# Kernel tuning notes

Measured on AMD Instinct MI355X. Metric: run time of the kernel, lower is better.

The kernel has to match this reference:

```python
import jax, jax.numpy as jnp
import numpy as np


def setup_inputs() -> dict:
    key = jax.random.key(0)
    k1, k2, k3 = jax.random.split(key, 3)
    B, C, D, H, W = 4, 64, 32, 64, 64
    x = jax.random.normal(k1, (B, C, D, H, W), dtype=jnp.float32)
    # Conv3d(in=2, out=1, k=7), PyTorch default init: U(-s, s), s = 1/sqrt(fan_in)
    fan_in = 2 * 7 * 7 * 7
    s = 1.0 / np.sqrt(fan_in)
    conv_w = jax.random.uniform(k2, (1, 2, 7, 7, 7), dtype=jnp.float32, minval=-s, maxval=s)
    conv_b = jax.random.uniform(k3, (1,), dtype=jnp.float32, minval=-s, maxval=s)
    return {"x": x, "conv_w": conv_w, "conv_b": conv_b}


def reference(x, conv_w, conv_b):
    # channel-wise max and mean -> [B, 2, D, H, W]
    xc = jnp.stack([jnp.max(x, axis=1), jnp.mean(x, axis=1)], axis=1)
    # conv3d 2->1, k7, stride 1, padding 3 (SAME)
    y = jax.lax.conv_general_dilated(
        xc, conv_w,
        window_strides=(1, 1, 1),
        padding=[(3, 3), (3, 3), (3, 3)],
        dimension_numbers=("NCDHW", "OIDHW", "NCDHW"),
    ) + conv_b[None, :, None, None, None]
    scale = jax.nn.sigmoid(y)  # [B, 1, D, H, W]
    return x * scale
```

## Files before the change

### kernel.cpp

```cpp
#include <hip/hip_runtime.h>
#include <math.h>

#define B_ 4
#define C_ 64
#define D_ 32
#define H_ 64
#define W_ 64
#define S_ (D_*H_*W_)
#define S4_ (S_/4)
#define HW_ (H_*W_)

typedef float floatx4 __attribute__((ext_vector_type(4)));

__global__ __launch_bounds__(256) void reduce_kernel(const float* __restrict__ x,
                                                     float* __restrict__ xc) {
    int i  = blockIdx.x * 256 + threadIdx.x;
    int b  = i >> 15;
    int s4 = i & (S4_ - 1);
    const float4* x4 = reinterpret_cast<const float4*>(x) + (size_t)b * C_ * S4_ + s4;
    float4 v = x4[0];
    float mx0 = v.x, mx1 = v.y, mx2 = v.z, mx3 = v.w;
    float sm0 = v.x, sm1 = v.y, sm2 = v.z, sm3 = v.w;
    #pragma unroll 8
    for (int c = 1; c < C_; ++c) {
        float4 t = x4[(size_t)c * S4_];
        mx0 = fmaxf(mx0, t.x); sm0 += t.x;
        mx1 = fmaxf(mx1, t.y); sm1 += t.y;
        mx2 = fmaxf(mx2, t.z); sm2 += t.z;
        mx3 = fmaxf(mx3, t.w); sm3 += t.w;
    }
    float4* o = reinterpret_cast<float4*>(xc);
    float4 a; a.x = mx0; a.y = mx1; a.z = mx2; a.w = mx3;
    o[((size_t)b * 2 + 0) * S4_ + s4] = a;
    const float inv = 1.0f / 64.0f;
    float4 m; m.x = sm0 * inv; m.y = sm1 * inv; m.z = sm2 * inv; m.w = sm3 * inv;
    o[((size_t)b * 2 + 1) * S4_ + s4] = m;
}

#define TZ 10
#define TY 14
#define TXS 72
#define PLANE (TY*TXS)
#define CHSZ (TZ*PLANE)
#define HALO_N (2*TZ*TY*70)

__global__ __launch_bounds__(256, 1) void conv_gate_kernel(const float* __restrict__ xc,
                                                           const float* __restrict__ x,
                                                           const float* __restrict__ cw,
                                                           const float* __restrict__ cb,
                                                           float* __restrict__ out) {
    __shared__ __align__(16) float tile[2 * CHSZ];

    const int tid = threadIdx.x;
    const int b  = blockIdx.z >> 3;
    const int d0 = (blockIdx.z & 7) * 4;
    const int h0 = blockIdx.y * 8;

    const int w4 = tid & 15;
    const int hh = (tid >> 4) & 7;
    const int dd = tid >> 7;
    const int dbase = d0 + 2 * dd;

    for (int base = tid; base < HALO_N; base += 256 * 8) {
        float sv[8];
        int   sa[8];
        #pragma unroll
        for (int k = 0; k < 8; ++k) {
            int idx = base + k * 256;
            sv[k] = 0.f;
            sa[k] = -1;
            if (idx < HALO_N) {
                int ch = idx / 9800;
                int r  = idx - ch * 9800;
                int z  = r / 980;
                int r2 = r - z * 980;
                int y  = r2 / 70;
                int xw = r2 - y * 70;
                sa[k] = ch * CHSZ + z * PLANE + y * TXS + xw;
                int gd = d0 + z - 3, gh = h0 + y - 3, gw = xw - 3;
                if ((unsigned)gd < (unsigned)D_ && (unsigned)gh < (unsigned)H_ &&
                    (unsigned)gw < (unsigned)W_)
                    sv[k] = xc[(size_t)(b * 2 + ch) * S_ + gd * HW_ + gh * W_ + gw];
            }
        }
        #pragma unroll
        for (int k = 0; k < 8; ++k)
            if (sa[k] >= 0) tile[sa[k]] = sv[k];
    }

    const int h = h0 + hh, w = w4 * 4;
    const size_t sp = (size_t)dbase * HW_ + (size_t)h * W_ + w;
    const float* xp = x + (size_t)b * C_ * S_ + sp;
    float* op = out + (size_t)b * C_ * S_ + sp;
    floatx4 v0[16];
    #pragma unroll
    for (int k = 0; k < 8; ++k) {
        const size_t off = (size_t)k * S_;
        v0[2 * k]     = *reinterpret_cast<const floatx4*>(xp + off);
        v0[2 * k + 1] = *reinterpret_cast<const floatx4*>(xp + off + HW_);
    }

    __syncthreads();

    float acc0[4] = {0.f, 0.f, 0.f, 0.f};
    float acc1[4] = {0.f, 0.f, 0.f, 0.f};
    for (int ch = 0; ch < 2; ++ch) {
        const float* tch = &tile[ch * CHSZ + 2 * dd * PLANE + w4 * 4];
        const float* wch = cw + ch * 343;
        for (int ky = 0; ky < 7; ++ky) {
            const float* trow = tch + (hh + ky) * TXS;
            const float* wky  = wch + ky * 7;
            float wp[7];
            #pragma unroll
            for (int z = 0; z < 8; ++z) {
                const float* rp = trow + z * PLANE;
                float4 f0 = *reinterpret_cast<const float4*>(rp);
                float4 f1 = *reinterpret_cast<const float4*>(rp + 4);
                float2 f2 = *reinterpret_cast<const float2*>(rp + 8);
                float win[10] = {f0.x, f0.y, f0.z, f0.w,
                                 f1.x, f1.y, f1.z, f1.w, f2.x, f2.y};
                if (z >= 1) {
                    #pragma unroll
                    for (int kw = 0; kw < 7; ++kw) {
                        acc1[0] = fmaf(win[kw + 0], wp[kw], acc1[0]);
                        acc1[1] = fmaf(win[kw + 1], wp[kw], acc1[1]);
                        acc1[2] = fmaf(win[kw + 2], wp[kw], acc1[2]);
                        acc1[3] = fmaf(win[kw + 3], wp[kw], acc1[3]);
                    }
                }
                if (z < 7) {
                    const float* wr = wky + z * 49;
                    float wc[7];
                    #pragma unroll
                    for (int k = 0; k < 7; ++k) wc[k] = wr[k];
                    #pragma unroll
                    for (int kw = 0; kw < 7; ++kw) {
                        acc0[0] = fmaf(win[kw + 0], wc[kw], acc0[0]);
                        acc0[1] = fmaf(win[kw + 1], wc[kw], acc0[1]);
                        acc0[2] = fmaf(win[kw + 2], wc[kw], acc0[2]);
                        acc0[3] = fmaf(win[kw + 3], wc[kw], acc0[3]);
                    }
                    #pragma unroll
                    for (int k = 0; k < 7; ++k) wp[k] = wc[k];
                }
            }
        }
    }

    const float bias = cb[0];
    floatx4 s0, s1;
    s0.x = 1.0f / (1.0f + __expf(-(acc0[0] + bias)));
    s0.y = 1.0f / (1.0f + __expf(-(acc0[1] + bias)));
    s0.z = 1.0f / (1.0f + __expf(-(acc0[2] + bias)));
    s0.w = 1.0f / (1.0f + __expf(-(acc0[3] + bias)));
    s1.x = 1.0f / (1.0f + __expf(-(acc1[0] + bias)));
    s1.y = 1.0f / (1.0f + __expf(-(acc1[1] + bias)));
    s1.z = 1.0f / (1.0f + __expf(-(acc1[2] + bias)));
    s1.w = 1.0f / (1.0f + __expf(-(acc1[3] + bias)));

    #pragma unroll
    for (int k = 0; k < 8; ++k) {
        const size_t off = (size_t)k * S_;
        *reinterpret_cast<floatx4*>(op + off)       = v0[2 * k] * s0;
        *reinterpret_cast<floatx4*>(op + off + HW_) = v0[2 * k + 1] * s1;
    }
    for (int c = 8; c < C_; c += 8) {
        floatx4 v[16];
        #pragma unroll
        for (int k = 0; k < 8; ++k) {
            const size_t off = (size_t)(c + k) * S_;
            v[2 * k]     = *reinterpret_cast<const floatx4*>(xp + off);
            v[2 * k + 1] = *reinterpret_cast<const floatx4*>(xp + off + HW_);
        }
        #pragma unroll
        for (int k = 0; k < 8; ++k) {
            const size_t off = (size_t)(c + k) * S_;
            *reinterpret_cast<floatx4*>(op + off)       = v[2 * k] * s0;
            *reinterpret_cast<floatx4*>(op + off + HW_) = v[2 * k + 1] * s1;
        }
    }
}

extern "C" void kernel_launch(void* const* d_in, const int* in_sizes, int n_in,
                              void* d_out, int out_size, void* d_ws, size_t ws_size,
                              hipStream_t stream) {
    const float* x  = (const float*)d_in[0];
    const float* cw = (const float*)d_in[1];
    const float* cb = (const float*)d_in[2];
    float* out = (float*)d_out;
    float* xc  = (float*)d_ws;

    reduce_kernel<<<dim3((B_ * S4_) / 256), dim3(256), 0, stream>>>(x, xc);
    conv_gate_kernel<<<dim3(1, H_ / 8, B_ * (D_ / 4)), dim3(256), 0, stream>>>(
        xc, x, cw, cb, out);
}
```

Baseline: 87.22 us.

## Halve depth per block in conv-gate kernel to double grid size

Each block now covers 2 depth slices instead of 4, with one output row per thread. This drops the two-accumulator z-reuse scheme and doubles the number of blocks from 256 to 512, so all CUs get work. The shared halo tile shrinks from 10 to 8 planes and launch bounds now allow 2 blocks per CU, which should raise occupancy and overlap of the memory-bound gating stream. In exchange the halo is re-read proportionally more often, and weight reuse across adjacent depths is lost.

```diff
diff --git a/kernel.cpp b/kernel.cpp
--- a/kernel.cpp
+++ b/kernel.cpp
@@ -37,14 +37,14 @@
     o[((size_t)b * 2 + 1) * S4_ + s4] = m;
 }
 
-#define TZ 10
-#define TY 14
-#define TXS 72
-#define PLANE (TY*TXS)
-#define CHSZ (TZ*PLANE)
-#define HALO_N (2*TZ*TY*70)
+#define ZT 8
+#define YT 14
+#define XS 72
+#define PLANE (YT*XS)
+#define CHSZ (ZT*PLANE)
+#define HALO_N (2*ZT*YT*70)
 
-__global__ __launch_bounds__(256, 1) void conv_gate_kernel(const float* __restrict__ xc,
+__global__ __launch_bounds__(256, 2) void conv_gate_kernel(const float* __restrict__ xc,
                                                            const float* __restrict__ x,
                                                            const float* __restrict__ cw,
                                                            const float* __restrict__ cb,
@@ -52,14 +52,13 @@
     __shared__ __align__(16) float tile[2 * CHSZ];
 
     const int tid = threadIdx.x;
-    const int b  = blockIdx.z >> 3;
-    const int d0 = (blockIdx.z & 7) * 4;
+    const int b  = blockIdx.z >> 4;
+    const int d0 = (blockIdx.z & 15) * 2;
     const int h0 = blockIdx.y * 8;
 
     const int w4 = tid & 15;
     const int hh = (tid >> 4) & 7;
     const int dd = tid >> 7;
-    const int dbase = d0 + 2 * dd;
 
     for (int base = tid; base < HALO_N; base += 256 * 8) {
         float sv[8];
@@ -70,13 +69,13 @@
             sv[k] = 0.f;
             sa[k] = -1;
             if (idx < HALO_N) {
-                int ch = idx / 9800;
-                int r  = idx - ch * 9800;
+                int ch = idx / 7840;
+                int r  = idx - ch * 7840;
                 int z  = r / 980;
                 int r2 = r - z * 980;
                 int y  = r2 / 70;
                 int xw = r2 - y * 70;
-                sa[k] = ch * CHSZ + z * PLANE + y * TXS + xw;
+                sa[k] = ch * CHSZ + z * PLANE + y * XS + xw;
                 int gd = d0 + z - 3, gh = h0 + y - 3, gw = xw - 3;
                 if ((unsigned)gd < (unsigned)D_ && (unsigned)gh < (unsigned)H_ &&
                     (unsigned)gw < (unsigned)W_)
@@ -89,95 +88,64 @@
     }
 
     const int h = h0 + hh, w = w4 * 4;
-    const size_t sp = (size_t)dbase * HW_ + (size_t)h * W_ + w;
+    const size_t sp = (size_t)(d0 + dd) * HW_ + (size_t)h * W_ + w;
     const float* xp = x + (size_t)b * C_ * S_ + sp;
     float* op = out + (size_t)b * C_ * S_ + sp;
     floatx4 v0[16];
     #pragma unroll
-    for (int k = 0; k < 8; ++k) {
-        const size_t off = (size_t)k * S_;
-        v0[2 * k]     = *reinterpret_cast<const floatx4*>(xp + off);
-        v0[2 * k + 1] = *reinterpret_cast<const floatx4*>(xp + off + HW_);
-    }
+    for (int k = 0; k < 16; ++k)
+        v0[k] = *reinterpret_cast<const floatx4*>(xp + (size_t)k * S_);
 
     __syncthreads();
 
-    float acc0[4] = {0.f, 0.f, 0.f, 0.f};
-    float acc1[4] = {0.f, 0.f, 0.f, 0.f};
+    float acc[4] = {0.f, 0.f, 0.f, 0.f};
     for (int ch = 0; ch < 2; ++ch) {
-        const float* tch = &tile[ch * CHSZ + 2 * dd * PLANE + w4 * 4];
+        const float* tch = &tile[ch * CHSZ + dd * PLANE + w4 * 4];
         const float* wch = cw + ch * 343;
         for (int ky = 0; ky < 7; ++ky) {
-            const float* trow = tch + (hh + ky) * TXS;
+            const float* trow = tch + (hh + ky) * XS;
             const float* wky  = wch + ky * 7;
-            float wp[7];
             #pragma unroll
-            for (int z = 0; z < 8; ++z) {
-                const float* rp = trow + z * PLANE;
+            for (int kz = 0; kz < 7; ++kz) {
+                const float* rp = trow + kz * PLANE;
                 float4 f0 = *reinterpret_cast<const float4*>(rp);
                 float4 f1 = *reinterpret_cast<const float4*>(rp + 4);
                 float2 f2 = *reinterpret_cast<const float2*>(rp + 8);
                 float win[10] = {f0.x, f0.y, f0.z, f0.w,
                                  f1.x, f1.y, f1.z, f1.w, f2.x, f2.y};
-                if (z >= 1) {
-                    #pragma unroll
-                    for (int kw = 0; kw < 7; ++kw) {
-                        acc1[0] = fmaf(win[kw + 0], wp[kw], acc1[0]);
-                        acc1[1] = fmaf(win[kw + 1], wp[kw], acc1[1]);
-                        acc1[2] = fmaf(win[kw + 2], wp[kw], acc1[2]);
-                        acc1[3] = fmaf(win[kw + 3], wp[kw], acc1[3]);
-                    }
-                }
-                if (z < 7) {
-                    const float* wr = wky + z * 49;
-                    float wc[7];
-                    #pragma unroll
-                    for (int k = 0; k < 7; ++k) wc[k] = wr[k];
-                    #pragma unroll
-                    for (int kw = 0; kw < 7; ++kw) {
-                        acc0[0] = fmaf(win[kw + 0], wc[kw], acc0[0]);
-                        acc0[1] = fmaf(win[kw + 1], wc[kw], acc0[1]);
-                        acc0[2] = fmaf(win[kw + 2], wc[kw], acc0[2]);
-                        acc0[3] = fmaf(win[kw + 3], wc[kw], acc0[3]);
-                    }
-                    #pragma unroll
-                    for (int k = 0; k < 7; ++k) wp[k] = wc[k];
+                const float* wr = wky + kz * 49;
+                float wc[7];
+                #pragma unroll
+                for (int k = 0; k < 7; ++k) wc[k] = wr[k];
+                #pragma unroll
+                for (int kw = 0; kw < 7; ++kw) {
+                    acc[0] = fmaf(win[kw + 0], wc[kw], acc[0]);
+                    acc[1] = fmaf(win[kw + 1], wc[kw], acc[1]);
+                    acc[2] = fmaf(win[kw + 2], wc[kw], acc[2]);
+                    acc[3] = fmaf(win[kw + 3], wc[kw], acc[3]);
                 }
             }
         }
     }
 
     const float bias = cb[0];
-    floatx4 s0, s1;
-    s0.x = 1.0f / (1.0f + __expf(-(acc0[0] + bias)));
-    s0.y = 1.0f / (1.0f + __expf(-(acc0[1] + bias)));
-    s0.z = 1.0f / (1.0f + __expf(-(acc0[2] + bias)));
-    s0.w = 1.0f / (1.0f + __expf(-(acc0[3] + bias)));
-    s1.x = 1.0f / (1.0f + __expf(-(acc1[0] + bias)));
-    s1.y = 1.0f / (1.0f + __expf(-(acc1[1] + bias)));
-    s1.z = 1.0f / (1.0f + __expf(-(acc1[2] + bias)));
-    s1.w = 1.0f / (1.0f + __expf(-(acc1[3] + bias)));
+    floatx4 s0;
+    s0.x = 1.0f / (1.0f + __expf(-(acc[0] + bias)));
+    s0.y = 1.0f / (1.0f + __expf(-(acc[1] + bias)));
+    s0.z = 1.0f / (1.0f + __expf(-(acc[2] + bias)));
+    s0.w = 1.0f / (1.0f + __expf(-(acc[3] + bias)));
 
     #pragma unroll
-    for (int k = 0; k < 8; ++k) {
-        const size_t off = (size_t)k * S_;
-        *reinterpret_cast<floatx4*>(op + off)       = v0[2 * k] * s0;
-        *reinterpret_cast<floatx4*>(op + off + HW_) = v0[2 * k + 1] * s1;
-    }
-    for (int c = 8; c < C_; c += 8) {
+    for (int k = 0; k < 16; ++k)
+        *reinterpret_cast<floatx4*>(op + (size_t)k * S_) = v0[k] * s0;
+    for (int c = 16; c < C_; c += 16) {
         floatx4 v[16];
         #pragma unroll
-        for (int k = 0; k < 8; ++k) {
-            const size_t off = (size_t)(c + k) * S_;
-            v[2 * k]     = *reinterpret_cast<const floatx4*>(xp + off);
-            v[2 * k + 1] = *reinterpret_cast<const floatx4*>(xp + off + HW_);
-        }
+        for (int k = 0; k < 16; ++k)
+            v[k] = *reinterpret_cast<const floatx4*>(xp + (size_t)(c + k) * S_);
         #pragma unroll
-        for (int k = 0; k < 8; ++k) {
-            const size_t off = (size_t)(c + k) * S_;
-            *reinterpret_cast<floatx4*>(op + off)       = v[2 * k] * s0;
-            *reinterpret_cast<floatx4*>(op + off + HW_) = v[2 * k + 1] * s1;
-        }
+        for (int k = 0; k < 16; ++k)
+            *reinterpret_cast<floatx4*>(op + (size_t)(c + k) * S_) = v[k] * s0;
     }
 }
 
@@ -191,6 +159,6 @@
     float* xc  = (float*)d_ws;
 
     reduce_kernel<<<dim3((B_ * S4_) / 256), dim3(256), 0, stream>>>(x, xc);
-    conv_gate_kernel<<<dim3(1, H_ / 8, B_ * (D_ / 4)), dim3(256), 0, stream>>>(
+    conv_gate_kernel<<<dim3(1, H_ / 8, B_ * (D_ / 2)), dim3(256), 0, stream>>>(
         xc, x, cw, cb, out);
 }
```

Measured after the change: 85.20 us. -2.3%, faster.
